# Optimization experiments

Hardware: AMD Instinct MI355X
Metric: run time of the kernel (lower is better)

## Reference

```python
import jax, jax.numpy as jnp
import numpy as np
from jax import lax
from jax.scipy.special import logsumexp

B, L, D = 64, 256, 512
NUM_CLASS, NREF, NNEG = 10, 50, 100
BLUR = 0.05
EPS_FINAL = BLUR ** 2  # geomloss: eps = blur**p with p=2
MARGIN = 10.0

# epsilon-scaling schedule (geomloss anneals eps geometrically, scaling=0.5),
# then extra iterations at the final eps for convergence.
_sched = []
_e = 8.0
while _e > EPS_FINAL:
    _sched.append(_e)
    _e *= 0.5
_sched += [EPS_FINAL] * 15
EPS_SCHED = jnp.asarray(np.array(_sched, np.float32))


def _cost(x, y):
    # geomloss p=2 cost: |x - y|^2 / 2   -> [N, M]
    return 0.5 * (jnp.sum(x * x, -1)[:, None] + jnp.sum(y * y, -1)[None, :] - 2.0 * (x @ y.T))


def _ot(a, x, b, y):
    """Entropic OT value <a,f>+<b,g> via log-domain Sinkhorn with eps-scaling.
    a,b are (possibly zero-padded) weights; x,y point clouds."""
    C = _cost(x, y)
    loga = jnp.where(a > 0, jnp.log(jnp.maximum(a, 1e-30)), -1e9)
    logb = jnp.where(b > 0, jnp.log(jnp.maximum(b, 1e-30)), -1e9)

    def body(fg, eps):
        f, g = fg
        f = -eps * logsumexp(logb[None, :] + (g[None, :] - C) / eps, axis=1)
        g = -eps * logsumexp(loga[:, None] + (f[:, None] - C) / eps, axis=0)
        return (f, g), None

    (f, g), _ = lax.scan(body, (jnp.zeros_like(a), jnp.zeros_like(b)), EPS_SCHED)
    return jnp.sum(a * f) + jnp.sum(b * g)


def _forward(anchor, weight, anchor_out_neg, t0, grade, grade_neg):
    Cn = t0.shape[0]
    w_ref = jnp.full((t0.shape[1],), 1.0 / t0.shape[1], anchor.dtype)
    w_neg = jnp.full((anchor_out_neg.shape[1],), 1.0 / anchor_out_neg.shape[1], anchor.dtype)

    # cross OT anchor_i vs every class reference cloud: [B, C]
    ot_cross = jax.vmap(lambda a, x: jax.vmap(lambda y: _ot(a, x, w_ref, y))(t0))(weight, anchor)
    # self terms for debiasing
    ot_aa = jax.vmap(lambda a, x: _ot(a, x, a, x))(weight, anchor)            # [B]
    ot_tt = jax.vmap(lambda y: _ot(w_ref, y, w_ref, y))(t0)                    # [C]
    ot_nn = jax.vmap(lambda y: _ot(w_neg, y, w_neg, y))(anchor_out_neg)        # [B]

    # debiased Sinkhorn divergence S = OT_ab - 0.5 OT_aa - 0.5 OT_bb
    S = ot_cross - 0.5 * ot_aa[:, None] - 0.5 * ot_tt[None, :]                 # [B, C]
    pos = jnp.take_along_axis(S, grade[:, None], axis=1)[:, 0]                 # [B]

    # after the torch k-loop, k == num_class-1 (loop-variable leak) -> t0[last]
    t_last = t0[Cn - 1]
    ot_ln = jax.vmap(lambda y: _ot(w_ref, t_last, w_neg, y))(anchor_out_neg)   # [B]
    S_last = ot_ln - 0.5 * ot_tt[Cn - 1] - 0.5 * ot_nn

    t_g = t0[grade_neg]                                                        # [B, NREF, D]
    ot_gn = jax.vmap(lambda yt, yn: _ot(w_ref, yt, w_neg, yn))(t_g, anchor_out_neg)
    S_gn = ot_gn - 0.5 * ot_tt[grade_neg] - 0.5 * ot_nn

    # hinge over all classes k != grade[i], plus the neg-cloud entry (index -1)
    notself = jnp.arange(Cn)[None, :] != grade[:, None]
    hinge_cls = jnp.sum(jnp.where(notself, jax.nn.relu(pos[:, None] - S + MARGIN), 0.0), axis=1)
    hinge_neg = jax.nn.relu(pos - S_last + MARGIN)
    loss_dif = jnp.abs(S_gn - S_last)
    return jnp.mean(hinge_cls + hinge_neg + loss_dif)


def setup_inputs() -> dict:
    key = jax.random.key(0)
    ks = jax.random.split(key, 7)
    anchor = jax.random.normal(ks[0], (B, L, D), jnp.float32)
    length_anchor = jax.random.randint(ks[1], (B,), L // 2, L + 1)
    grade = jax.random.randint(ks[2], (B,), 0, NUM_CLASS)
    w = jax.random.uniform(ks[3], (B, L), jnp.float32, 1e-3, 1.0)
    mask = jnp.arange(L)[None, :] < length_anchor[:, None]
    w = w * mask
    weight = w / jnp.sum(w, axis=1, keepdims=True)  # normalized histogram per sample
    anchor_out_neg = jax.random.normal(ks[4], (B, NNEG, D), jnp.float32)
    grade_neg = jax.random.randint(ks[5], (B,), 0, NUM_CLASS)
    t0 = jax.random.normal(ks[6], (NUM_CLASS, NREF, D), jnp.float32)
    return {"anchor": anchor, "length_anchor": length_anchor, "grade": grade,
            "weight": weight, "anchor_out_neg": anchor_out_neg,
            "grade_neg": grade_neg, "t0": t0, "num_class": NUM_CLASS}


def reference(anchor, length_anchor, grade, weight, anchor_out_neg, grade_neg, t0, num_class):
    # length_anchor is encoded in the zero-padding of `weight` (masked positions
    # have weight 0 and drop out of the OT); num_class == t0.shape[0].
    return _forward(anchor, weight, anchor_out_neg, t0, grade, grade_neg)
```

## Files before the change

kernel.cpp:

```cpp
#include <hip/hip_runtime.h>

#define NB   64
#define LA   256
#define DD   512
#define NCLS 10
#define NREF 50
#define NNEG 100
#define MARGIN 10.0f
#define NITER 27

#define LOG2E 1.44269504f
#define LN2   0.69314718f
#define LC50  (-3.9120230054f)
#define LC100 (-4.6051701860f)

#define OFF_CX   ((size_t)0)
#define SZ_CX    ((size_t)64*500*256)
#define OFF_CAA  (OFF_CX + SZ_CX)
#define SZ_CAA   ((size_t)64*256*256)
#define OFF_CNN  (OFF_CAA + SZ_CAA)
#define SZ_CNN   ((size_t)64*100*100)
#define OFF_CLN  (OFF_CNN + SZ_CNN)
#define SZ_CLN   ((size_t)64*50*100)
#define OFF_CGN  (OFF_CLN + SZ_CLN)
#define SZ_CGN   ((size_t)64*50*100)
#define OFF_CTT  (OFF_CGN + SZ_CGN)
#define SZ_CTT   ((size_t)10*50*50)
#define OFF_SQA  (OFF_CTT + SZ_CTT)
#define OFF_SQN  (OFF_SQA + (size_t)64*256)
#define OFF_SQT  (OFF_SQN + (size_t)64*100)
#define OFF_OTX  (OFF_SQT + (size_t)500)
#define OFF_OTAA (OFF_OTX + (size_t)640)
#define OFF_OTNN (OFF_OTAA + (size_t)64)
#define OFF_OTLN (OFF_OTNN + (size_t)64)
#define OFF_OTGN (OFF_OTLN + (size_t)64)
#define OFF_OTTT (OFF_OTGN + (size_t)64)

__device__ __forceinline__ float eps_at(int it) {
    return (it < 12) ? ldexpf(8.0f, -it) : 0.0025f;
}

__device__ __forceinline__ float block_sum256(float v, float* red, int tid) {
    #pragma unroll
    for (int off = 1; off < 64; off <<= 1) v += __shfl_xor(v, off);
    if ((tid & 63) == 0) red[tid >> 6] = v;
    __syncthreads();
    return red[0] + red[1] + red[2] + red[3];
}

__global__ __launch_bounds__(256) void sq_kernel(const float* __restrict__ anchor,
                                                 const float* __restrict__ neg,
                                                 const float* __restrict__ t0,
                                                 float* __restrict__ ws) {
    int gw   = (blockIdx.x * 256 + threadIdx.x) >> 6;
    int lane = threadIdx.x & 63;
    const int nA = NB * LA, nN = NB * NNEG, nT = NCLS * NREF;
    if (gw >= nA + nN + nT) return;
    const float* row; float* outp;
    if (gw < nA)           { row = anchor + (size_t)gw * DD;          outp = ws + OFF_SQA + gw; }
    else if (gw < nA + nN) { int r = gw - nA;      row = neg + (size_t)r * DD; outp = ws + OFF_SQN + r; }
    else                   { int r = gw - nA - nN; row = t0  + (size_t)r * DD; outp = ws + OFF_SQT + r; }
    const float4* r4 = (const float4*)row;
    float4 u = r4[lane * 2], v = r4[lane * 2 + 1];
    float s = u.x*u.x + u.y*u.y + u.z*u.z + u.w*u.w
            + v.x*v.x + v.y*v.y + v.z*v.z + v.w*v.w;
    #pragma unroll
    for (int off = 1; off < 64; off <<= 1) s += __shfl_xor(s, off);
    if (lane == 0) *outp = 0.5f * s;
}

#define CTM 128
#define CTK 16
__global__ __launch_bounds__(256) void cost128(const float* __restrict__ anchor,
                                               const float* __restrict__ neg,
                                               const float* __restrict__ t0,
                                               const int* __restrict__ gneg,
                                               float* __restrict__ ws) {
    __shared__ __align__(16) float As[CTK][CTM];
    __shared__ __align__(16) float Bs[CTK][CTM];
    int bid = blockIdx.x, tid = threadIdx.x;
    const float *X, *Y, *sqx, *sqy;
    float* Cout; int N, M, ldc, r0, c0;
    bool tr = false;
    if (bid < 512) {
        int b = bid >> 3, t = bid & 7;
        r0 = (t >> 2) * 128; c0 = (t & 3) * 128;
        X = anchor + (size_t)b * LA * DD; Y = t0; N = LA; M = 500; ldc = 500;
        Cout = ws + OFF_CX + (size_t)b * 500 * 256;
        sqx = ws + OFF_SQA + b * LA; sqy = ws + OFF_SQT;
        tr = true;
    } else if (bid < 768) {
        int b2 = bid - 512; int b = b2 >> 2, t = b2 & 3;
        r0 = (t >> 1) * 128; c0 = (t & 1) * 128;
        X = Y = anchor + (size_t)b * LA * DD; N = M = LA; ldc = LA;
        Cout = ws + OFF_CAA + (size_t)b * LA * LA;
        sqx = sqy = ws + OFF_SQA + b * LA;
    } else if (bid < 832) {
        int b = bid - 768; r0 = 0; c0 = 0;
        X = Y = neg + (size_t)b * NNEG * DD; N = M = NNEG; ldc = NNEG;
        Cout = ws + OFF_CNN + (size_t)b * NNEG * NNEG;
        sqx = sqy = ws + OFF_SQN + b * NNEG;
    } else if (bid < 896) {
        int b = bid - 832; r0 = 0; c0 = 0;
        X = t0 + (size_t)9 * NREF * DD; Y = neg + (size_t)b * NNEG * DD;
        N = NREF; M = NNEG; ldc = NNEG;
        Cout = ws + OFF_CLN + (size_t)b * NREF * NNEG;
        sqx = ws + OFF_SQT + 9 * NREF; sqy = ws + OFF_SQN + b * NNEG;
    } else if (bid < 960) {
        int b = bid - 896; r0 = 0; c0 = 0;
        int gc = gneg[b];
        X = t0 + (size_t)gc * NREF * DD; Y = neg + (size_t)b * NNEG * DD;
        N = NREF; M = NNEG; ldc = NNEG;
        Cout = ws + OFF_CGN + (size_t)b * NREF * NNEG;
        sqx = ws + OFF_SQT + gc * NREF; sqy = ws + OFF_SQN + b * NNEG;
    } else {
        int c = bid - 960; r0 = 0; c0 = 0;
        X = Y = t0 + (size_t)c * NREF * DD; N = M = NREF; ldc = NREF;
        Cout = ws + OFF_CTT + (size_t)c * NREF * NREF;
        sqx = sqy = ws + OFF_SQT + c * NREF;
    }
    int row = tid & 127, kq = tid >> 7;
    int tx = tid & 15, ty = tid >> 4;
    bool xok = (r0 + row) < N, yok = (c0 + row) < M;
    const float* xrow = X + (size_t)(r0 + row) * DD + kq * 8;
    const float* yrow = Y + (size_t)(c0 + row) * DD + kq * 8;
    float acc[8][8];
    #pragma unroll
    for (int a = 0; a < 8; a++)
        #pragma unroll
        for (int b = 0; b < 8; b++) acc[a][b] = 0.f;
    for (int k0 = 0; k0 < DD; k0 += CTK) {
        float4 xa0 = xok ? *(const float4*)(xrow + k0)     : make_float4(0,0,0,0);
        float4 xa1 = xok ? *(const float4*)(xrow + k0 + 4) : make_float4(0,0,0,0);
        float4 ya0 = yok ? *(const float4*)(yrow + k0)     : make_float4(0,0,0,0);
        float4 ya1 = yok ? *(const float4*)(yrow + k0 + 4) : make_float4(0,0,0,0);
        __syncthreads();
        int kb = kq * 8;
        As[kb+0][row]=xa0.x; As[kb+1][row]=xa0.y; As[kb+2][row]=xa0.z; As[kb+3][row]=xa0.w;
        As[kb+4][row]=xa1.x; As[kb+5][row]=xa1.y; As[kb+6][row]=xa1.z; As[kb+7][row]=xa1.w;
        Bs[kb+0][row]=ya0.x; Bs[kb+1][row]=ya0.y; Bs[kb+2][row]=ya0.z; Bs[kb+3][row]=ya0.w;
        Bs[kb+4][row]=ya1.x; Bs[kb+5][row]=ya1.y; Bs[kb+6][row]=ya1.z; Bs[kb+7][row]=ya1.w;
        __syncthreads();
        #pragma unroll
        for (int k = 0; k < CTK; k++) {
            float4 a0 = *(const float4*)&As[k][ty << 3];
            float4 a1 = *(const float4*)&As[k][(ty << 3) + 4];
            float4 b0 = *(const float4*)&Bs[k][tx << 3];
            float4 b1 = *(const float4*)&Bs[k][(tx << 3) + 4];
            float av[8] = {a0.x,a0.y,a0.z,a0.w,a1.x,a1.y,a1.z,a1.w};
            float bv[8] = {b0.x,b0.y,b0.z,b0.w,b1.x,b1.y,b1.z,b1.w};
            #pragma unroll
            for (int a = 0; a < 8; a++)
                #pragma unroll
                for (int b = 0; b < 8; b++)
                    acc[a][b] = fmaf(av[a], bv[b], acc[a][b]);
        }
    }
    #pragma unroll
    for (int a = 0; a < 8; a++) {
        int n = r0 + (ty << 3) + a;
        if (n < N) {
            float sx = sqx[n];
            #pragma unroll
            for (int b = 0; b < 8; b++) {
                int m = c0 + (tx << 3) + b;
                if (m < M) {
                    float v = sx + sqy[m] - acc[a][b];
                    if (tr) Cout[(size_t)m * 256 + n] = v;
                    else    Cout[(size_t)n * ldc + m] = v;
                }
            }
        }
    }
}

__global__ __launch_bounds__(1024) void sink_small(const float* __restrict__ weight,
                                                   float* __restrict__ ws) {
    __shared__ __align__(16) float smem[1056];
    int bid = blockIdx.x, tid = threadIdx.x;

    if (bid < 64) {
        float* ahp = smem;
        float* red = smem + 1024;
        int w = tid >> 6, lane = tid & 63;
        int c = (w << 4) | (lane & 15);
        int rg = lane >> 4;
        const float* Cg = ws + OFF_CAA + ((size_t)bid << 16);
        float Creg[64];
        #pragma unroll
        for (int k = 0; k < 64; ++k)
            Creg[k] = Cg[(size_t)((rg << 6) + k) * 256 + c];
        float wgt = weight[(size_t)bid * LA + c];
        float la = (wgt > 0.f) ? __logf(fmaxf(wgt, 1e-30f)) : -1e9f;
        float h = 0.f, fs = 0.f;
        int wseg = (c >> 6) * 68 + (c & 63);
        if (rg == 0) ahp[wseg] = 8.0f * la;
        __syncthreads();
        for (int app = 0; app < 54; ++app) {
            float eps = eps_at(app >> 1);
            const float4* a4 = (const float4*)(ahp + (app & 1) * 272 + rg * 68);
            float m0=-3.4e38f, m1=-3.4e38f, m2=-3.4e38f, m3=-3.4e38f;
            #pragma unroll
            for (int k = 0; k < 16; ++k) {
                float4 av = a4[k];
                m0 = fmaxf(m0, av.x - Creg[4*k+0]);
                m1 = fmaxf(m1, av.y - Creg[4*k+1]);
                m2 = fmaxf(m2, av.z - Creg[4*k+2]);
                m3 = fmaxf(m3, av.w - Creg[4*k+3]);
            }
            float m = fmaxf(fmaxf(m0, m1), fmaxf(m2, m3));
            m = fmaxf(m, __shfl_xor(m, 16));
            m = fmaxf(m, __shfl_xor(m, 32));
            float ie2 = (1.0f / eps) * LOG2E;
            float s0=0.f, s1=0.f, s2=0.f, s3=0.f;
            #pragma unroll
            for (int k = 0; k < 16; ++k) {
                float4 av = a4[k];
                s0 += exp2f((av.x - Creg[4*k+0] - m) * ie2);
                s1 += exp2f((av.y - Creg[4*k+1] - m) * ie2);
                s2 += exp2f((av.z - Creg[4*k+2] - m) * ie2);
                s3 += exp2f((av.w - Creg[4*k+3] - m) * ie2);
            }
            float s = (s0 + s1) + (s2 + s3);
            s += __shfl_xor(s, 16);
            s += __shfl_xor(s, 32);
            h = -fmaf(eps * LN2, __log2f(s), m);
            if (app == 52) fs = h;
            float epsn = eps_at((app + 1) >> 1);
            if (rg == 0) ahp[((app + 1) & 1) * 272 + wseg] = fmaf(epsn, la, h);
            __syncthreads();
        }
        float contrib = (rg == 0) ? wgt * (fs + h) : 0.f;
        #pragma unroll
        for (int off = 1; off < 64; off <<= 1) contrib += __shfl_xor(contrib, off);
        if (lane == 0) red[w] = contrib;
        __syncthreads();
        if (tid == 0) {
            float s = 0.f;
            #pragma unroll
            for (int k = 0; k < 16; ++k) s += red[k];
            ws[OFF_OTAA + bid] = s;
        }

    } else if (bid < 80) {
        int sub = tid >> 8, stid = tid & 255;
        int inst = ((bid - 64) << 2) | sub;
        const float* Cg = ws + OFF_CNN + (size_t)inst * 10000;
        float* S = smem + (sub << 8);
        bool act = stid < 200;
        int c = stid >> 1, rg = stid & 1;
        float Creg[52];
        if (act) {
            #pragma unroll
            for (int k = 0; k < 52; ++k) {
                int r = rg * 52 + k;
                Creg[k] = (r < 100) ? Cg[(size_t)r * 100 + c] : 3.0e30f;
            }
        }
        if (stid < 100) S[stid] = 8.0f * LC100;
        if (stid >= 100 && stid < 104) { S[stid] = -1.0e30f; S[104 + stid] = -1.0e30f; }
        __syncthreads();
        float h = 0.f, fs = 0.f;
        for (int app = 0; app < 54; ++app) {
            float eps = eps_at(app >> 1);
            if (act) {
                const float4* a4 = (const float4*)(S + (app & 1) * 104 + rg * 52);
                float m0=-3.4e38f, m1=-3.4e38f, m2=-3.4e38f, m3=-3.4e38f;
                #pragma unroll
                for (int k = 0; k < 13; ++k) {
                    float4 av = a4[k];
                    m0 = fmaxf(m0, av.x - Creg[4*k+0]);
                    m1 = fmaxf(m1, av.y - Creg[4*k+1]);
                    m2 = fmaxf(m2, av.z - Creg[4*k+2]);
                    m3 = fmaxf(m3, av.w - Creg[4*k+3]);
                }
                float m = fmaxf(fmaxf(m0, m1), fmaxf(m2, m3));
                m = fmaxf(m, __shfl_xor(m, 1));
                float ie2 = (1.0f / eps) * LOG2E;
                float s0=0.f, s1=0.f, s2=0.f, s3=0.f;
                #pragma unroll
                for (int k = 0; k < 13; ++k) {
                    float4 av = a4[k];
                    s0 += exp2f((av.x - Creg[4*k+0] - m) * ie2);
                    s1 += exp2f((av.y - Creg[4*k+1] - m) * ie2);
                    s2 += exp2f((av.z - Creg[4*k+2] - m) * ie2);
                    s3 += exp2f((av.w - Creg[4*k+3] - m) * ie2);
                }
                float s = (s0 + s1) + (s2 + s3);
                s += __shfl_xor(s, 1);
                h = -fmaf(eps * LN2, __log2f(s), m);
                if (app == 52) fs = h;
                float epsn = eps_at((app + 1) >> 1);
                if (rg == 0) S[((app + 1) & 1) * 104 + c] = fmaf(epsn, LC100, h);
            }
            __syncthreads();
        }
        float contrib = (act && rg == 0) ? 0.01f * (fs + h) : 0.f;
        #pragma unroll
        for (int off = 1; off < 64; off <<= 1) contrib += __shfl_xor(contrib, off);
        if ((tid & 63) == 0) smem[1024 + (tid >> 6)] = contrib;
        __syncthreads();
        if (stid == 0) {
            int b4 = 1024 + (sub << 2);
            ws[OFF_OTNN + inst] = smem[b4] + smem[b4+1] + smem[b4+2] + smem[b4+3];
        }

    } else if (bid < 112) {
        int sub = tid >> 8, stid = tid & 255;
        int inst = ((bid - 80) << 2) | sub;
        const float* Cg = (inst < 64) ? ws + OFF_CLN + (size_t)inst * 5000
                                      : ws + OFF_CGN + (size_t)(inst - 64) * 5000;
        float* outp = (inst < 64) ? ws + OFF_OTLN + inst : ws + OFF_OTGN + (inst - 64);
        float* S = smem + (sub << 8);
        float* gS = S;
        float* fS = S + 104;
        bool actf = stid < 100; int rf = stid >> 1, hf = stid & 1;
        bool actg = (stid >= 128) && (stid < 228); int cg = stid - 128;
        float Creg[52];
        if (actf) {
            #pragma unroll
            for (int k = 0; k < 52; ++k) {
                int cc = hf * 52 + k;
                Creg[k] = (cc < 100) ? Cg[(size_t)rf * 100 + cc] : 3.0e30f;
            }
        } else if (actg) {
            #pragma unroll
            for (int k = 0; k < 52; ++k)
                Creg[k] = (k < 50) ? Cg[(size_t)k * 100 + cg] : 3.0e30f;
        }
        if (stid < 104) gS[stid] = (stid < 100) ? 8.0f * LC100 : -1.0e30f;
        if (stid == 0) { fS[50] = -1.0e30f; fS[51] = -1.0e30f; }
        __syncthreads();
        float fr = 0.f, gr = 0.f;
        for (int it = 0; it < NITER; ++it) {
            float eps = eps_at(it), ie2 = (1.0f / eps) * LOG2E;
            if (actf) {
                const float4* g4 = (const float4*)(gS + hf * 52);
                float m0=-3.4e38f, m1=-3.4e38f, m2=-3.4e38f, m3=-3.4e38f;
                #pragma unroll
                for (int k = 0; k < 13; ++k) {
                    float4 gv = g4[k];
                    m0 = fmaxf(m0, gv.x - Creg[4*k+0]);
                    m1 = fmaxf(m1, gv.y - Creg[4*k+1]);
                    m2 = fmaxf(m2, gv.z - Creg[4*k+2]);
                    m3 = fmaxf(m3, gv.w - Creg[4*k+3]);
                }
                float m = fmaxf(fmaxf(m0, m1), fmaxf(m2, m3));
                m = fmaxf(m, __shfl_xor(m, 1));
                float s0=0.f, s1=0.f, s2=0.f, s3=0.f;
                #pragma unroll
                for (int k = 0; k < 13; ++k) {
                    float4 gv = g4[k];
                    s0 += exp2f((gv.x - Creg[4*k+0] - m) * ie2);
                    s1 += exp2f((gv.y - Creg[4*k+1] - m) * ie2);
                    s2 += exp2f((gv.z - Creg[4*k+2] - m) * ie2);
                    s3 += exp2f((gv.w - Creg[4*k+3] - m) * ie2);
                }
                float s = (s0 + s1) + (s2 + s3);
                s += __shfl_xor(s, 1);
                fr = -fmaf(eps * LN2, __log2f(s), m);
                if (hf == 0) fS[rf] = fmaf(eps, LC50, fr);
            }
            __syncthreads();
            if (actg) {
                const float4* f4 = (const float4*)fS;
                float m0=-3.4e38f, m1=-3.4e38f, m2=-3.4e38f, m3=-3.4e38f;
                #pragma unroll
                for (int k = 0; k < 13; ++k) {
                    float4 fv = f4[k];
                    m0 = fmaxf(m0, fv.x - Creg[4*k+0]);
                    m1 = fmaxf(m1, fv.y - Creg[4*k+1]);
                    m2 = fmaxf(m2, fv.z - Creg[4*k+2]);
                    m3 = fmaxf(m3, fv.w - Creg[4*k+3]);
                }
                float m = fmaxf(fmaxf(m0, m1), fmaxf(m2, m3));
                float s0=0.f, s1=0.f, s2=0.f, s3=0.f;
                #pragma unroll
                for (int k = 0; k < 13; ++k) {
                    float4 fv = f4[k];
                    s0 += exp2f((fv.x - Creg[4*k+0] - m) * ie2);
                    s1 += exp2f((fv.y - Creg[4*k+1] - m) * ie2);
                    s2 += exp2f((fv.z - Creg[4*k+2] - m) * ie2);
                    s3 += exp2f((fv.w - Creg[4*k+3] - m) * ie2);
                }
                gr = -fmaf(eps * LN2, __log2f((s0+s1)+(s2+s3)), m);
                float epsn = eps_at(it + 1);
                gS[cg] = fmaf(epsn, LC100, gr);
            }
            __syncthreads();
        }
        float contrib = 0.f;
        if (actf && hf == 0) contrib += 0.02f * fr;
        if (actg) contrib += 0.01f * gr;
        #pragma unroll
        for (int off = 1; off < 64; off <<= 1) contrib += __shfl_xor(contrib, off);
        if ((tid & 63) == 0) smem[1024 + (tid >> 6)] = contrib;
        __syncthreads();
        if (stid == 0) {
            int b4 = 1024 + (sub << 2);
            *outp = smem[b4] + smem[b4+1] + smem[b4+2] + smem[b4+3];
        }

    } else {
        int sub = tid >> 8, stid = tid & 255;
        int inst = ((bid - 112) << 2) | sub;
        bool live = inst < 10;
        const float* Cg = ws + OFF_CTT + (size_t)inst * 2500;
        float* S = smem + (sub << 8);
        bool act = live && (stid < 50);
        float Creg[52];
        if (act) {
            #pragma unroll
            for (int k = 0; k < 52; ++k)
                Creg[k] = (k < 50) ? Cg[(size_t)k * 50 + stid] : 3.0e30f;
        }
        if (live && stid < 50) S[stid] = 8.0f * LC50;
        if (live && stid >= 50 && stid < 52) { S[stid] = -1.0e30f; S[52 + stid] = -1.0e30f; }
        __syncthreads();
        float h = 0.f, fs = 0.f;
        for (int app = 0; app < 54; ++app) {
            float eps = eps_at(app >> 1);
            if (act) {
                const float4* a4 = (const float4*)(S + (app & 1) * 52);
                float m0=-3.4e38f, m1=-3.4e38f, m2=-3.4e38f, m3=-3.4e38f;
                #pragma unroll
                for (int k = 0; k < 13; ++k) {
                    float4 av = a4[k];
                    m0 = fmaxf(m0, av.x - Creg[4*k+0]);
                    m1 = fmaxf(m1, av.y - Creg[4*k+1]);
                    m2 = fmaxf(m2, av.z - Creg[4*k+2]);
                    m3 = fmaxf(m3, av.w - Creg[4*k+3]);
                }
                float m = fmaxf(fmaxf(m0, m1), fmaxf(m2, m3));
                float ie2 = (1.0f / eps) * LOG2E;
                float s0=0.f, s1=0.f, s2=0.f, s3=0.f;
                #pragma unroll
                for (int k = 0; k < 13; ++k) {
                    float4 av = a4[k];
                    s0 += exp2f((av.x - Creg[4*k+0] - m) * ie2);
                    s1 += exp2f((av.y - Creg[4*k+1] - m) * ie2);
                    s2 += exp2f((av.z - Creg[4*k+2] - m) * ie2);
                    s3 += exp2f((av.w - Creg[4*k+3] - m) * ie2);
                }
                h = -fmaf(eps * LN2, __log2f((s0+s1)+(s2+s3)), m);
                if (app == 52) fs = h;
                float epsn = eps_at((app + 1) >> 1);
                S[((app + 1) & 1) * 52 + stid] = fmaf(epsn, LC50, h);
            }
            __syncthreads();
        }
        float contrib = act ? 0.02f * (fs + h) : 0.f;
        #pragma unroll
        for (int off = 1; off < 64; off <<= 1) contrib += __shfl_xor(contrib, off);
        if ((tid & 63) == 0) smem[1024 + (tid >> 6)] = contrib;
        __syncthreads();
        if (stid == 0 && live) {
            int b4 = 1024 + (sub << 2);
            ws[OFF_OTTT + inst] = smem[b4] + smem[b4+1] + smem[b4+2] + smem[b4+3];
        }
    }
}

__global__ __launch_bounds__(256, 3) void sink_cross(const float* __restrict__ weight,
                                                     float* __restrict__ ws) {
    __shared__ __align__(16) float smem[13324];
    float* red = smem + 13320;
    int bid = blockIdx.x, tid = threadIdx.x;
    int i = bid / 10, c = bid - i * 10;
    float* CsT = smem;
    float* agS = smem + 13000;
    float* gSp = smem + 13260;
    const float* Cgbase = ws + OFF_CX + (size_t)i * (500 * 256) + (size_t)c * (50 * 256);
    for (int e = tid; e < 3200; e += 256) {
        int r = e >> 6, n4 = (e & 63) << 2;
        *(float4*)&CsT[r * 260 + n4] = *(const float4*)&Cgbase[(size_t)e << 2];
    }
    float w = weight[(size_t)i * LA + tid];
    float la_r = (w > 0.f) ? __logf(fmaxf(w, 1e-30f)) : -1e9f;
    if (tid < 52) gSp[tid] = (tid < 50) ? 0.f : -1.0e30f;
    __syncthreads();
    float Creg[52];
    #pragma unroll
    for (int r = 0; r < 52; ++r) Creg[r] = (r < 50) ? CsT[r * 260 + tid] : 3.0e30f;
    int grp = tid >> 4, j = tid & 15;
    for (int it = 0; it < NITER; ++it) {
        float eps = eps_at(it), ie2 = (1.0f / eps) * LOG2E;
        {
            const float4* g4 = (const float4*)gSp;
            float m0=-3.4e38f, m1=-3.4e38f, m2=-3.4e38f, m3=-3.4e38f;
            #pragma unroll
            for (int k = 0; k < 13; ++k) {
                float4 gv = g4[k];
                m0 = fmaxf(m0, gv.x - Creg[4*k+0]);
                m1 = fmaxf(m1, gv.y - Creg[4*k+1]);
                m2 = fmaxf(m2, gv.z - Creg[4*k+2]);
                m3 = fmaxf(m3, gv.w - Creg[4*k+3]);
            }
            float m = fmaxf(fmaxf(m0, m1), fmaxf(m2, m3));
            float s0=0.f, s1=0.f, s2=0.f, s3=0.f;
            #pragma unroll
            for (int k = 0; k < 13; ++k) {
                float4 gv = g4[k];
                s0 += exp2f((gv.x - Creg[4*k+0] - m) * ie2);
                s1 += exp2f((gv.y - Creg[4*k+1] - m) * ie2);
                s2 += exp2f((gv.z - Creg[4*k+2] - m) * ie2);
                s3 += exp2f((gv.w - Creg[4*k+3] - m) * ie2);
            }
            float L = fmaf(eps * LN2, __log2f((s0+s1)+(s2+s3)), m);
            float f = -fmaf(eps, LC50, L);
            agS[tid] = fmaf(eps, la_r, f);
        }
        __syncthreads();
        float4 agr[4];
        #pragma unroll
        for (int q = 0; q < 4; ++q)
            agr[q] = *(const float4*)&agS[(j << 2) + (q << 6)];
        for (int o = grp; o < 50; o += 16) {
            const float* Cr = &CsT[o * 260];
            float u[16];
            #pragma unroll
            for (int q = 0; q < 4; ++q) {
                float4 cv = *(const float4*)&Cr[(j << 2) + (q << 6)];
                u[4*q+0] = agr[q].x - cv.x;
                u[4*q+1] = agr[q].y - cv.y;
                u[4*q+2] = agr[q].z - cv.z;
                u[4*q+3] = agr[q].w - cv.w;
            }
            float a0 = fmaxf(fmaxf(u[0], u[4]),  fmaxf(u[8],  u[12]));
            float a1 = fmaxf(fmaxf(u[1], u[5]),  fmaxf(u[9],  u[13]));
            float a2 = fmaxf(fmaxf(u[2], u[6]),  fmaxf(u[10], u[14]));
            float a3 = fmaxf(fmaxf(u[3], u[7]),  fmaxf(u[11], u[15]));
            float m = fmaxf(fmaxf(a0, a1), fmaxf(a2, a3));
            #pragma unroll
            for (int off = 1; off < 16; off <<= 1) m = fmaxf(m, __shfl_xor(m, off));
            float s0=0.f, s1=0.f, s2=0.f, s3=0.f;
            #pragma unroll
            for (int k = 0; k < 16; ++k) {
                float e = exp2f((u[k] - m) * ie2);
                if ((k & 3) == 0) s0 += e;
                else if ((k & 3) == 1) s1 += e;
                else if ((k & 3) == 2) s2 += e;
                else s3 += e;
            }
            float s = (s0 + s1) + (s2 + s3);
            #pragma unroll
            for (int off = 1; off < 16; off <<= 1) s += __shfl_xor(s, off);
            if (j == 0) gSp[o] = -fmaf(eps * LN2, __log2f(s), m);
        }
        __syncthreads();
    }
    float f_t = agS[tid] - 0.0025f * la_r;
    float contrib = w * f_t + (tid < 50 ? 0.02f * gSp[tid] : 0.f);
    contrib = block_sum256(contrib, red, tid);
    if (tid == 0) ws[OFF_OTX + bid] = contrib;
}

__global__ void assemble_kernel(const int* __restrict__ grade, const int* __restrict__ gneg,
                                const float* __restrict__ ws, float* __restrict__ out) {
    int i = threadIdx.x;
    float total = 0.f;
    if (i < 64) {
        float aa  = ws[OFF_OTAA + i];
        float nn  = ws[OFF_OTNN + i];
        float lnv = ws[OFF_OTLN + i];
        float gnv = ws[OFF_OTGN + i];
        int g  = grade[i];
        int gi = gneg[i];
        float tt9 = ws[OFF_OTTT + 9];
        float ttg = ws[OFF_OTTT + gi];
        float Slast = lnv - 0.5f * tt9 - 0.5f * nn;
        float Sgn   = gnv - 0.5f * ttg - 0.5f * nn;
        float Sv[10];
        #pragma unroll
        for (int k = 0; k < 10; k++)
            Sv[k] = ws[OFF_OTX + i * 10 + k] - 0.5f * aa - 0.5f * ws[OFF_OTTT + k];
        float pos = 0.f;
        #pragma unroll
        for (int k = 0; k < 10; k++) pos = (k == g) ? Sv[k] : pos;
        float hc = 0.f;
        #pragma unroll
        for (int k = 0; k < 10; k++)
            if (k != g) hc += fmaxf(pos - Sv[k] + MARGIN, 0.f);
        float hn = fmaxf(pos - Slast + MARGIN, 0.f);
        total = hc + hn + fabsf(Sgn - Slast);
    }
    #pragma unroll
    for (int off = 1; off < 64; off <<= 1) total += __shfl_xor(total, off);
    if (i == 0) out[0] = total * (1.0f / 64.0f);
}

extern "C" void kernel_launch(void* const* d_in, const int* in_sizes, int n_in,
                              void* d_out, int out_size, void* d_ws, size_t ws_size,
                              hipStream_t stream) {
    const float* anchor = (const float*)d_in[0];
    const int*   grade  = (const int*)d_in[2];
    const float* weight = (const float*)d_in[3];
    const float* neg    = (const float*)d_in[4];
    const int*   gneg   = (const int*)d_in[5];
    const float* t0     = (const float*)d_in[6];
    float* ws  = (float*)d_ws;
    float* out = (float*)d_out;

    sq_kernel      <<<5821, 256, 0, stream>>>(anchor, neg, t0, ws);
    cost128        <<<970, 256, 0, stream>>>(anchor, neg, t0, gneg, ws);
    sink_small     <<<115, 1024, 0, stream>>>(weight, ws);
    sink_cross     <<<640, 256, 0, stream>>>(weight, ws);
    assemble_kernel<<<1, 64, 0, stream>>>(grade, gneg, ws, out);
}
```

Before: 721.4 us.

## Fuse cross Sinkhorn solves into small-solve kernel to overlap tails

Merges the separate sink_cross launch into the sink_small kernel as extra blocks. Each new 1024-thread block runs two cross OT instances, 512 threads each, with 256 active per instance. The aim is to fill CUs left idle by the few long-running small-solve blocks and to drop one launch boundary. In exchange, shared memory grows to about 106KB per block and half the threads in the cross blocks sit idle. Occupancy for the cross work also drops compared with the old 256-thread, 3-blocks-per-CU layout.

```diff
diff --git a/kernel.cpp b/kernel.cpp
--- a/kernel.cpp
+++ b/kernel.cpp
@@ -38,14 +38,6 @@
 
 __device__ __forceinline__ float eps_at(int it) {
     return (it < 12) ? ldexpf(8.0f, -it) : 0.0025f;
-}
-
-__device__ __forceinline__ float block_sum256(float v, float* red, int tid) {
-    #pragma unroll
-    for (int off = 1; off < 64; off <<= 1) v += __shfl_xor(v, off);
-    if ((tid & 63) == 0) red[tid >> 6] = v;
-    __syncthreads();
-    return red[0] + red[1] + red[2] + red[3];
 }
 
 __global__ __launch_bounds__(256) void sq_kernel(const float* __restrict__ anchor,
@@ -174,9 +166,9 @@
     }
 }
 
-__global__ __launch_bounds__(1024) void sink_small(const float* __restrict__ weight,
+__global__ __launch_bounds__(1024) void sink_fused(const float* __restrict__ weight,
                                                    float* __restrict__ ws) {
-    __shared__ __align__(16) float smem[1056];
+    __shared__ __align__(16) float smem[26664];
     int bid = blockIdx.x, tid = threadIdx.x;
 
     if (bid < 64) {
@@ -401,7 +393,7 @@
             *outp = smem[b4] + smem[b4+1] + smem[b4+2] + smem[b4+3];
         }
 
-    } else {
+    } else if (bid < 115) {
         int sub = tid >> 8, stid = tid & 255;
         int inst = ((bid - 112) << 2) | sub;
         bool live = inst < 10;
@@ -458,101 +450,122 @@
             int b4 = 1024 + (sub << 2);
             ws[OFF_OTTT + inst] = smem[b4] + smem[b4+1] + smem[b4+2] + smem[b4+3];
         }
+
+    } else {
+        int sub = tid >> 9, stid = tid & 511;
+        int inst = ((bid - 115) << 1) | sub;
+        int i = inst / 10, c = inst - i * 10;
+        float* base = smem + sub * 13324;
+        float* CsT = base;
+        float* agS = base + 13000;
+        float* gSp = base + 13260;
+        float* red = smem + 26648;
+        const float* Cgbase = ws + OFF_CX + (size_t)i * (500 * 256) + (size_t)c * (50 * 256);
+        bool wk = stid < 256;
+        if (wk) {
+            for (int e = stid; e < 3200; e += 256) {
+                int r = e >> 6, n4 = (e & 63) << 2;
+                *(float4*)&CsT[r * 260 + n4] = *(const float4*)&Cgbase[(size_t)e << 2];
+            }
+        }
+        float w = 0.f, la_r = 0.f;
+        if (wk) {
+            w = weight[(size_t)i * LA + stid];
+            la_r = (w > 0.f) ? __logf(fmaxf(w, 1e-30f)) : -1e9f;
+            if (stid < 52) gSp[stid] = (stid < 50) ? 0.f : -1.0e30f;
+        }
+        __syncthreads();
+        float Creg[52];
+        if (wk) {
+            #pragma unroll
+            for (int r = 0; r < 52; ++r) Creg[r] = (r < 50) ? CsT[r * 260 + stid] : 3.0e30f;
+        }
+        int grp = stid >> 4, j = stid & 15;
+        for (int it = 0; it < NITER; ++it) {
+            float eps = eps_at(it), ie2 = (1.0f / eps) * LOG2E;
+            if (wk) {
+                const float4* g4 = (const float4*)gSp;
+                float m0=-3.4e38f, m1=-3.4e38f, m2=-3.4e38f, m3=-3.4e38f;
+                #pragma unroll
+                for (int k = 0; k < 13; ++k) {
+                    float4 gv = g4[k];
+                    m0 = fmaxf(m0, gv.x - Creg[4*k+0]);
+                    m1 = fmaxf(m1, gv.y - Creg[4*k+1]);
+                    m2 = fmaxf(m2, gv.z - Creg[4*k+2]);
+                    m3 = fmaxf(m3, gv.w - Creg[4*k+3]);
+                }
+                float m = fmaxf(fmaxf(m0, m1), fmaxf(m2, m3));
+                float s0=0.f, s1=0.f, s2=0.f, s3=0.f;
+                #pragma unroll
+                for (int k = 0; k < 13; ++k) {
+                    float4 gv = g4[k];
+                    s0 += exp2f((gv.x - Creg[4*k+0] - m) * ie2);
+                    s1 += exp2f((gv.y - Creg[4*k+1] - m) * ie2);
+                    s2 += exp2f((gv.z - Creg[4*k+2] - m) * ie2);
+                    s3 += exp2f((gv.w - Creg[4*k+3] - m) * ie2);
+                }
+                float L = fmaf(eps * LN2, __log2f((s0+s1)+(s2+s3)), m);
+                float f = -fmaf(eps, LC50, L);
+                agS[stid] = fmaf(eps, la_r, f);
+            }
+            __syncthreads();
+            if (wk) {
+                float4 agr[4];
+                #pragma unroll
+                for (int q = 0; q < 4; ++q)
+                    agr[q] = *(const float4*)&agS[(j << 2) + (q << 6)];
+                for (int o = grp; o < 50; o += 16) {
+                    const float* Cr = &CsT[o * 260];
+                    float u[16];
+                    #pragma unroll
+                    for (int q = 0; q < 4; ++q) {
+                        float4 cv = *(const float4*)&Cr[(j << 2) + (q << 6)];
+                        u[4*q+0] = agr[q].x - cv.x;
+                        u[4*q+1] = agr[q].y - cv.y;
+                        u[4*q+2] = agr[q].z - cv.z;
+                        u[4*q+3] = agr[q].w - cv.w;
+                    }
+                    float a0 = fmaxf(fmaxf(u[0], u[4]),  fmaxf(u[8],  u[12]));
+                    float a1 = fmaxf(fmaxf(u[1], u[5]),  fmaxf(u[9],  u[13]));
+                    float a2 = fmaxf(fmaxf(u[2], u[6]),  fmaxf(u[10], u[14]));
+                    float a3 = fmaxf(fmaxf(u[3], u[7]),  fmaxf(u[11], u[15]));
+                    float m = fmaxf(fmaxf(a0, a1), fmaxf(a2, a3));
+                    #pragma unroll
+                    for (int off = 1; off < 16; off <<= 1) m = fmaxf(m, __shfl_xor(m, off));
+                    float s0=0.f, s1=0.f, s2=0.f, s3=0.f;
+                    #pragma unroll
+                    for (int k = 0; k < 16; ++k) {
+                        float e = exp2f((u[k] - m) * ie2);
+                        if ((k & 3) == 0) s0 += e;
+                        else if ((k & 3) == 1) s1 += e;
+                        else if ((k & 3) == 2) s2 += e;
+                        else s3 += e;
+                    }
+                    float s = (s0 + s1) + (s2 + s3);
+                    #pragma unroll
+                    for (int off = 1; off < 16; off <<= 1) s += __shfl_xor(s, off);
+                    if (j == 0) gSp[o] = -fmaf(eps * LN2, __log2f(s), m);
+                }
+            }
+            __syncthreads();
+        }
+        float contrib = 0.f;
+        if (wk) {
+            float f_t = agS[stid] - 0.0025f * la_r;
+            contrib = w * f_t + (stid < 50 ? 0.02f * gSp[stid] : 0.f);
+        }
+        #pragma unroll
+        for (int off = 1; off < 64; off <<= 1) contrib += __shfl_xor(contrib, off);
+        if ((tid & 63) == 0) red[tid >> 6] = contrib;
+        __syncthreads();
+        if (stid == 0) {
+            int b8 = sub << 3;
+            float s = 0.f;
+            #pragma unroll
+            for (int k = 0; k < 4; ++k) s += red[b8 + k];
+            ws[OFF_OTX + inst] = s;
+        }
     }
-}
-
-__global__ __launch_bounds__(256, 3) void sink_cross(const float* __restrict__ weight,
-                                                     float* __restrict__ ws) {
-    __shared__ __align__(16) float smem[13324];
-    float* red = smem + 13320;
-    int bid = blockIdx.x, tid = threadIdx.x;
-    int i = bid / 10, c = bid - i * 10;
-    float* CsT = smem;
-    float* agS = smem + 13000;
-    float* gSp = smem + 13260;
-    const float* Cgbase = ws + OFF_CX + (size_t)i * (500 * 256) + (size_t)c * (50 * 256);
-    for (int e = tid; e < 3200; e += 256) {
-        int r = e >> 6, n4 = (e & 63) << 2;
-        *(float4*)&CsT[r * 260 + n4] = *(const float4*)&Cgbase[(size_t)e << 2];
-    }
-    float w = weight[(size_t)i * LA + tid];
-    float la_r = (w > 0.f) ? __logf(fmaxf(w, 1e-30f)) : -1e9f;
-    if (tid < 52) gSp[tid] = (tid < 50) ? 0.f : -1.0e30f;
-    __syncthreads();
-    float Creg[52];
-    #pragma unroll
-    for (int r = 0; r < 52; ++r) Creg[r] = (r < 50) ? CsT[r * 260 + tid] : 3.0e30f;
-    int grp = tid >> 4, j = tid & 15;
-    for (int it = 0; it < NITER; ++it) {
-        float eps = eps_at(it), ie2 = (1.0f / eps) * LOG2E;
-        {
-            const float4* g4 = (const float4*)gSp;
-            float m0=-3.4e38f, m1=-3.4e38f, m2=-3.4e38f, m3=-3.4e38f;
-            #pragma unroll
-            for (int k = 0; k < 13; ++k) {
-                float4 gv = g4[k];
-                m0 = fmaxf(m0, gv.x - Creg[4*k+0]);
-                m1 = fmaxf(m1, gv.y - Creg[4*k+1]);
-                m2 = fmaxf(m2, gv.z - Creg[4*k+2]);
-                m3 = fmaxf(m3, gv.w - Creg[4*k+3]);
-            }
-            float m = fmaxf(fmaxf(m0, m1), fmaxf(m2, m3));
-            float s0=0.f, s1=0.f, s2=0.f, s3=0.f;
-            #pragma unroll
-            for (int k = 0; k < 13; ++k) {
-                float4 gv = g4[k];
-                s0 += exp2f((gv.x - Creg[4*k+0] - m) * ie2);
-                s1 += exp2f((gv.y - Creg[4*k+1] - m) * ie2);
-                s2 += exp2f((gv.z - Creg[4*k+2] - m) * ie2);
-                s3 += exp2f((gv.w - Creg[4*k+3] - m) * ie2);
-            }
-            float L = fmaf(eps * LN2, __log2f((s0+s1)+(s2+s3)), m);
-            float f = -fmaf(eps, LC50, L);
-            agS[tid] = fmaf(eps, la_r, f);
-        }
-        __syncthreads();
-        float4 agr[4];
-        #pragma unroll
-        for (int q = 0; q < 4; ++q)
-            agr[q] = *(const float4*)&agS[(j << 2) + (q << 6)];
-        for (int o = grp; o < 50; o += 16) {
-            const float* Cr = &CsT[o * 260];
-            float u[16];
-            #pragma unroll
-            for (int q = 0; q < 4; ++q) {
-                float4 cv = *(const float4*)&Cr[(j << 2) + (q << 6)];
-                u[4*q+0] = agr[q].x - cv.x;
-                u[4*q+1] = agr[q].y - cv.y;
-                u[4*q+2] = agr[q].z - cv.z;
-                u[4*q+3] = agr[q].w - cv.w;
-            }
-            float a0 = fmaxf(fmaxf(u[0], u[4]),  fmaxf(u[8],  u[12]));
-            float a1 = fmaxf(fmaxf(u[1], u[5]),  fmaxf(u[9],  u[13]));
-            float a2 = fmaxf(fmaxf(u[2], u[6]),  fmaxf(u[10], u[14]));
-            float a3 = fmaxf(fmaxf(u[3], u[7]),  fmaxf(u[11], u[15]));
-            float m = fmaxf(fmaxf(a0, a1), fmaxf(a2, a3));
-            #pragma unroll
-            for (int off = 1; off < 16; off <<= 1) m = fmaxf(m, __shfl_xor(m, off));
-            float s0=0.f, s1=0.f, s2=0.f, s3=0.f;
-            #pragma unroll
-            for (int k = 0; k < 16; ++k) {
-                float e = exp2f((u[k] - m) * ie2);
-                if ((k & 3) == 0) s0 += e;
-                else if ((k & 3) == 1) s1 += e;
-                else if ((k & 3) == 2) s2 += e;
-                else s3 += e;
-            }
-            float s = (s0 + s1) + (s2 + s3);
-            #pragma unroll
-            for (int off = 1; off < 16; off <<= 1) s += __shfl_xor(s, off);
-            if (j == 0) gSp[o] = -fmaf(eps * LN2, __log2f(s), m);
-        }
-        __syncthreads();
-    }
-    float f_t = agS[tid] - 0.0025f * la_r;
-    float contrib = w * f_t + (tid < 50 ? 0.02f * gSp[tid] : 0.f);
-    contrib = block_sum256(contrib, red, tid);
-    if (tid == 0) ws[OFF_OTX + bid] = contrib;
 }
 
 __global__ void assemble_kernel(const int* __restrict__ grade, const int* __restrict__ gneg,
@@ -603,7 +616,6 @@
 
     sq_kernel      <<<5821, 256, 0, stream>>>(anchor, neg, t0, ws);
     cost128        <<<970, 256, 0, stream>>>(anchor, neg, t0, gneg, ws);
-    sink_small     <<<115, 1024, 0, stream>>>(weight, ws);
-    sink_cross     <<<640, 256, 0, stream>>>(weight, ws);
+    sink_fused     <<<435, 1024, 0, stream>>>(weight, ws);
     assemble_kernel<<<1, 64, 0, stream>>>(grade, gneg, ws, out);
 }
```

New measurement: 591.2 us (median of 2 runs). 1.22x faster.
